# Performance work log

Hardware: AMD Instinct MI355X
Metric: run time of the kernel (lower is better)

Reference implementation:

```python
import jax, jax.numpy as jnp
import numpy as np
from jax import lax

DIM = 64
NUM_EXPERTS = 6
TOP_K = 2
B, H, W = 8, 128, 128
DN = ('NCHW', 'OIHW', 'NCHW')


def setup_inputs() -> dict:
    key = jax.random.key(0)
    ks = jax.random.split(key, 8)
    s_in = 1.0 / np.sqrt(DIM * 9)
    s_r = 1.0 / np.sqrt(DIM)
    return {
        'x': jax.random.normal(ks[0], (B, DIM, H, W), jnp.float32),
        'router_w': jax.random.normal(ks[1], (NUM_EXPERTS, DIM), jnp.float32) * s_r,
        'router_b': jnp.zeros((NUM_EXPERTS,), jnp.float32),
        'expert_bias': jnp.zeros((NUM_EXPERTS,), jnp.float32),
        'w1': jax.random.normal(ks[2], (NUM_EXPERTS, DIM, DIM, 3, 3), jnp.float32) * s_in,
        'b1': jnp.zeros((NUM_EXPERTS, DIM), jnp.float32),
        'w2': jax.random.normal(ks[3], (NUM_EXPERTS, DIM, DIM, 3, 3), jnp.float32) * s_in,
        'b2': jnp.zeros((NUM_EXPERTS, DIM), jnp.float32),
    }


def reference(x, router_w, router_b, expert_bias, w1, b1, w2, b2):
    # ---- router: global avg pool -> linear -> clamp -> +bias -> softmax ----
    pooled = x.mean(axis=(2, 3))                               # [B, C]
    logits = pooled @ router_w.T + router_b                    # [B, E]
    logits = jnp.clip(logits, -10.0, 10.0) + expert_bias[None, :]
    probs = jnp.clip(jax.nn.softmax(logits, axis=1), 1e-6, 1.0)
    top_v, top_i = lax.top_k(probs, TOP_K)                     # [B, K]
    top_v = top_v / (top_v.sum(axis=1, keepdims=True) + 1e-8)
    # per-sample combine weight for each expert: sum of top-k probs routed to it
    w_be = (jax.nn.one_hot(top_i, NUM_EXPERTS, dtype=x.dtype) * top_v[..., None]).sum(axis=1)  # [B, E]

    # ---- experts: Conv3x3 -> GELU -> Conv3x3, vmapped over expert dim ----
    def expert(w1e, b1e, w2e, b2e):
        h = lax.conv_general_dilated(x, w1e, (1, 1), 'SAME', dimension_numbers=DN)
        h = jax.nn.gelu(h + b1e[None, :, None, None])
        h = lax.conv_general_dilated(h, w2e, (1, 1), 'SAME', dimension_numbers=DN)
        return h + b2e[None, :, None, None]

    ys = jax.vmap(expert)(w1, b1, w2, b2)                      # [E, B, C, H, W]
    out = jnp.einsum('be,ebchw->bchw', w_be, ys)
    return out, jnp.zeros((), x.dtype)
```

## Files before the change

### kernel.cpp

```cpp
#include <hip/hip_runtime.h>
#include <hip/hip_bf16.h>
#include <cstdint>

typedef __attribute__((ext_vector_type(8))) short sh8;
typedef __attribute__((ext_vector_type(16))) float f32x16;
typedef unsigned short ushort_t;

#define HH 128
#define WW 128
#define HWSZ (HH*WW)
#define PW 130
#define PW64 (PW*64)
#define IMGSZ ((size_t)PW*PW*64)
#define WBEXP 36864

__device__ __forceinline__ float gelu_tanh(float x) {
    float u = 0.7978845608028654f * (x + 0.044715f * x * x * x);
    return 0.5f * x * (1.0f + tanhf(u));
}
__device__ __forceinline__ ushort_t f2b(float f) {
    __hip_bfloat16 h = __float2bfloat16(f);
    return *reinterpret_cast<ushort_t*>(&h);
}
__device__ __forceinline__ f32x16 mfma_bf16(sh8 a, sh8 b, f32x16 c) {
    return __builtin_amdgcn_mfma_f32_32x32x16_bf16(a, b, c, 0, 0, 0);
}

__global__ __launch_bounds__(256) void pool_kernel(const float* __restrict__ x,
                                                   float* __restrict__ pooled) {
    int bc = blockIdx.x;
    const float4* p4 = reinterpret_cast<const float4*>(x + (size_t)bc * HWSZ);
    float s = 0.f;
    for (int i = threadIdx.x; i < HWSZ / 4; i += 256) {
        float4 v = p4[i];
        s += (v.x + v.y) + (v.z + v.w);
    }
#pragma unroll
    for (int off = 32; off > 0; off >>= 1) s += __shfl_down(s, off, 64);
    __shared__ float red[4];
    if ((threadIdx.x & 63) == 0) red[threadIdx.x >> 6] = s;
    __syncthreads();
    if (threadIdx.x == 0)
        pooled[bc] = (red[0] + red[1] + red[2] + red[3]) * (1.0f / (float)HWSZ);
}

__global__ __launch_bounds__(64) void router_kernel(const float* __restrict__ pooled,
                                                    const float* __restrict__ rw,
                                                    const float* __restrict__ rb,
                                                    const float* __restrict__ eb,
                                                    const float* __restrict__ b2,
                                                    int* __restrict__ topi,
                                                    float* __restrict__ topw,
                                                    float* __restrict__ bsum,
                                                    float* __restrict__ outz) {
    __shared__ int sti[16];
    __shared__ float stw[16];
    int b = threadIdx.x;
    if (b == 8) outz[(size_t)8 * 64 * HWSZ] = 0.f;
    if (b < 8) {
        float lg[6];
        for (int e = 0; e < 6; ++e) {
            float s = rb[e];
            for (int c = 0; c < 64; ++c) s += pooled[b * 64 + c] * rw[e * 64 + c];
            lg[e] = fminf(fmaxf(s, -10.f), 10.f) + eb[e];
        }
        float m = lg[0];
        for (int e = 1; e < 6; ++e) m = fmaxf(m, lg[e]);
        float den = 0.f, pr[6];
        for (int e = 0; e < 6; ++e) { pr[e] = expf(lg[e] - m); den += pr[e]; }
        float inv = 1.0f / den;
        for (int e = 0; e < 6; ++e) pr[e] = fminf(fmaxf(pr[e] * inv, 1e-6f), 1.0f);
        int i0 = 0; float v0 = pr[0];
        for (int e = 1; e < 6; ++e) if (pr[e] > v0) { v0 = pr[e]; i0 = e; }
        int i1 = -1; float v1 = -1.f;
        for (int e = 0; e < 6; ++e) { if (e == i0) continue; if (pr[e] > v1) { v1 = pr[e]; i1 = e; } }
        float s2 = v0 + v1 + 1e-8f;
        topi[b * 2 + 0] = i0; topi[b * 2 + 1] = i1;
        topw[b * 2 + 0] = v0 / s2; topw[b * 2 + 1] = v1 / s2;
        sti[b * 2 + 0] = i0; sti[b * 2 + 1] = i1;
        stw[b * 2 + 0] = v0 / s2; stw[b * 2 + 1] = v1 / s2;
    }
    __syncthreads();
    for (int i = threadIdx.x; i < 512; i += 64) {
        int bb = i >> 6, c = i & 63;
        bsum[i] = stw[bb * 2] * b2[sti[bb * 2] * 64 + c] +
                  stw[bb * 2 + 1] * b2[sti[bb * 2 + 1] * 64 + c];
    }
}

__global__ __launch_bounds__(256) void convx_kernel(const float* __restrict__ x,
                                                    ushort_t* __restrict__ xp) {
    __shared__ ushort_t lt[128][72];
    int b = blockIdx.x >> 7, h = blockIdx.x & 127;
    int tid = threadIdx.x;
#pragma unroll
    for (int k = 0; k < 8; ++k) {
        int idx = tid + k * 256;
        int ci = idx >> 5, wg = idx & 31;
        float4 v = *reinterpret_cast<const float4*>(
            x + ((size_t)b * 64 + ci) * HWSZ + (size_t)h * WW + wg * 4);
        lt[wg * 4 + 0][ci] = f2b(v.x);
        lt[wg * 4 + 1][ci] = f2b(v.y);
        lt[wg * 4 + 2][ci] = f2b(v.z);
        lt[wg * 4 + 3][ci] = f2b(v.w);
    }
    __syncthreads();
    int w = tid >> 1, half = tid & 1;
    const int4* src = reinterpret_cast<const int4*>(&lt[w][half * 32]);
    int4 a0 = src[0], a1 = src[1], a2 = src[2], a3 = src[3];
    int4* dst = reinterpret_cast<int4*>(
        xp + (((size_t)b * PW + (h + 1)) * PW + (w + 1)) * 64 + half * 32);
    dst[0] = a0; dst[1] = a1; dst[2] = a2; dst[3] = a3;
}

__global__ __launch_bounds__(256) void convw1_kernel(const float* __restrict__ w1,
                                                     ushort_t* __restrict__ wb1f) {
    int blk = blockIdx.x;
    int e = blk / 9, t = blk - e * 9;
    for (int idx = threadIdx.x; idx < 4096; idx += 256) {
        int kc = idx >> 10, n = (idx >> 9) & 1, l = (idx >> 3) & 63, j = idx & 7;
        int co = n * 32 + (l & 31);
        int ci = kc * 16 + (l >> 5) * 8 + j;
        wb1f[(size_t)e * WBEXP + t * 4096 + idx] =
            f2b(w1[(((size_t)e * 64 + co) * 64 + ci) * 9 + t]);
    }
}

__global__ __launch_bounds__(256) void convw2_kernel(const float* __restrict__ w2,
                                                     const int* __restrict__ topi,
                                                     const float* __restrict__ topw,
                                                     ushort_t* __restrict__ wb2f) {
    int blk = blockIdx.x;
    int bs = blk / 9, t = blk - bs * 9;
    int e = topi[bs];
    float cw = topw[bs];
    for (int idx = threadIdx.x; idx < 4096; idx += 256) {
        int kc = idx >> 10, n = (idx >> 9) & 1, l = (idx >> 3) & 63, j = idx & 7;
        int co = n * 32 + (l & 31);
        int ci = kc * 16 + (l >> 5) * 8 + j;
        wb2f[(size_t)bs * WBEXP + t * 4096 + idx] =
            f2b(cw * w2[(((size_t)e * 64 + co) * 64 + ci) * 9 + t]);
    }
}

__global__ __launch_bounds__(256) void halo_kernel(ushort_t* __restrict__ buf) {
    ushort_t* p = buf + (size_t)blockIdx.x * IMGSZ;
    int tid = threadIdx.x;
    int4 z = make_int4(0, 0, 0, 0);
    for (int i = tid; i < 1040; i += 256) {
        reinterpret_cast<int4*>(p)[i] = z;
        reinterpret_cast<int4*>(p + (size_t)129 * PW64)[i] = z;
    }
    for (int i = tid; i < 128 * 8; i += 256) {
        int row = 1 + (i >> 3), j = i & 7;
        reinterpret_cast<int4*>(p + (size_t)row * PW64)[j] = z;
        reinterpret_cast<int4*>(p + ((size_t)row * PW + 129) * 64)[j] = z;
    }
}

__global__ __launch_bounds__(256) void conv1_mfma(const ushort_t* __restrict__ xp,
                                                  const ushort_t* __restrict__ wb1f,
                                                  const float* __restrict__ b1,
                                                  const int* __restrict__ topi,
                                                  ushort_t* __restrict__ hp,
                                                  int nslots, int slot0) {
    const int z = blockIdx.z;
    const int b = z / nslots, sl = z - b * nslots, s = slot0 + sl;
    const int e = topi[b * 2 + s];
    const int tid = threadIdx.x, l = tid & 63, wid = tid >> 6;
    const int n = wid & 1, rp = wid >> 1;
    const int hgrp = blockIdx.x >> 2, w0 = (blockIdx.x & 3) * 32;
    const int l31 = l & 31, lh = l >> 5;
    const int h0 = hgrp * 8 + rp * 4;

    const ushort_t* wbW = wb1f + (size_t)e * WBEXP + n * 512 + l * 8;
    const ushort_t* aB = xp + (size_t)b * IMGSZ + (size_t)h0 * PW64 +
                         (size_t)w0 * 64 + l31 * 64 + lh * 8;

    f32x16 acc0, acc1, acc2, acc3;
#pragma unroll
    for (int k2 = 0; k2 < 16; ++k2) { acc0[k2] = 0.f; acc1[k2] = 0.f; acc2[k2] = 0.f; acc3[k2] = 0.f; }

#pragma unroll
    for (int dr = 0; dr < 3; ++dr) {
        const ushort_t* ar = aB + (size_t)dr * PW64;
#pragma unroll
        for (int dc = 0; dc < 3; ++dc) {
            const ushort_t* ap = ar + dc * 64;
            const int t = dr * 3 + dc;
#pragma unroll
            for (int kc = 0; kc < 4; ++kc) {
                sh8 bf = *reinterpret_cast<const sh8*>(wbW + ((size_t)(t * 4 + kc)) * 1024);
                sh8 a0 = *reinterpret_cast<const sh8*>(ap + kc * 16);
                sh8 a1 = *reinterpret_cast<const sh8*>(ap + PW64 + kc * 16);
                sh8 a2 = *reinterpret_cast<const sh8*>(ap + 2 * PW64 + kc * 16);
                sh8 a3 = *reinterpret_cast<const sh8*>(ap + 3 * PW64 + kc * 16);
                acc0 = mfma_bf16(a0, bf, acc0);
                acc1 = mfma_bf16(a1, bf, acc1);
                acc2 = mfma_bf16(a2, bf, acc2);
                acc3 = mfma_bf16(a3, bf, acc3);
            }
        }
    }

    const float bv = b1[e * 64 + n * 32 + l31];
    const size_t ob0 = (((size_t)(sl * 8 + b) * PW + (h0 + 1)) * PW + (w0 + 1)) * 64 + n * 32 + l31;
#pragma unroll
    for (int i = 0; i < 4; ++i) {
        f32x16 a = (i == 0) ? acc0 : (i == 1) ? acc1 : (i == 2) ? acc2 : acc3;
        const size_t ob = ob0 + (size_t)i * PW64;
#pragma unroll
        for (int r = 0; r < 16; ++r) {
            int px = (r & 3) + 8 * (r >> 2) + 4 * lh;
            hp[ob + (size_t)px * 64] = f2b(gelu_tanh(a[r] + bv));
        }
    }
}

__global__ __launch_bounds__(256) void conv2_mfma(const ushort_t* __restrict__ hp,
                                                  const ushort_t* __restrict__ wb2f,
                                                  const float* __restrict__ bsum,
                                                  float* __restrict__ outF,
                                                  int s0, int s1, int addmode) {
    __shared__ float lt[4][32][33];
    const int b = blockIdx.z;
    const int tid = threadIdx.x, l = tid & 63, wid = tid >> 6;
    const int n = wid & 1, rp = wid >> 1;
    const int hgrp = blockIdx.x >> 2, w0 = (blockIdx.x & 3) * 32;
    const int l31 = l & 31, lh = l >> 5;
    const int h0 = hgrp * 4 + rp * 2;

    f32x16 acc0, acc1;
#pragma unroll
    for (int k2 = 0; k2 < 16; ++k2) { acc0[k2] = 0.f; acc1[k2] = 0.f; }

    for (int s = s0; s <= s1; ++s) {
        const ushort_t* wbW = wb2f + (size_t)(b * 2 + s) * WBEXP + n * 512 + l * 8;
        const ushort_t* aB = hp + (size_t)((s - s0) * 8 + b) * IMGSZ + (size_t)h0 * PW64 +
                             (size_t)w0 * 64 + l31 * 64 + lh * 8;
#pragma unroll
        for (int dr = 0; dr < 3; ++dr) {
            const ushort_t* ar = aB + (size_t)dr * PW64;
#pragma unroll
            for (int dc = 0; dc < 3; ++dc) {
                const ushort_t* ap = ar + dc * 64;
                const int t = dr * 3 + dc;
#pragma unroll
                for (int kc = 0; kc < 4; ++kc) {
                    sh8 bf = *reinterpret_cast<const sh8*>(wbW + ((size_t)(t * 4 + kc)) * 1024);
                    sh8 a0 = *reinterpret_cast<const sh8*>(ap + kc * 16);
                    sh8 a1 = *reinterpret_cast<const sh8*>(ap + PW64 + kc * 16);
                    acc0 = mfma_bf16(a0, bf, acc0);
                    acc1 = mfma_bf16(a1, bf, acc1);
                }
            }
        }
    }

    const float bq = addmode ? 0.f : bsum[b * 64 + n * 32 + l31];
#pragma unroll
    for (int i = 0; i < 2; ++i) {
        f32x16 a = i ? acc1 : acc0;
        const int h = h0 + i;
#pragma unroll
        for (int r = 0; r < 16; ++r) {
            int px = (r & 3) + 8 * (r >> 2) + 4 * lh;
            lt[wid][px][l31] = a[r] + bq;
        }
        const int q = lh, co = l31;
        const size_t ob = ((size_t)(b * 64 + n * 32 + co)) * HWSZ + (size_t)h * WW + w0 + q * 16;
#pragma unroll
        for (int v = 0; v < 4; ++v) {
            float o0 = lt[wid][q * 16 + v * 4 + 0][co];
            float o1 = lt[wid][q * 16 + v * 4 + 1][co];
            float o2 = lt[wid][q * 16 + v * 4 + 2][co];
            float o3 = lt[wid][q * 16 + v * 4 + 3][co];
            float4* dst = reinterpret_cast<float4*>(outF + ob + v * 4);
            if (addmode) {
                float4 pv = *dst;
                o0 += pv.x; o1 += pv.y; o2 += pv.z; o3 += pv.w;
            }
            float4 o; o.x = o0; o.y = o1; o.z = o2; o.w = o3;
            *dst = o;
        }
    }
}

extern "C" void kernel_launch(void* const* d_in, const int* in_sizes, int n_in,
                              void* d_out, int out_size, void* d_ws, size_t ws_size,
                              hipStream_t stream) {
    const float* x  = (const float*)d_in[0];
    const float* rw = (const float*)d_in[1];
    const float* rb = (const float*)d_in[2];
    const float* eb = (const float*)d_in[3];
    const float* w1 = (const float*)d_in[4];
    const float* b1 = (const float*)d_in[5];
    const float* w2 = (const float*)d_in[6];
    const float* b2 = (const float*)d_in[7];
    float* out = (float*)d_out;

    char* ws = (char*)d_ws;
    float*    pooled = (float*)(ws + 0);
    int*      topi   = (int*)(ws + 2048);
    float*    topw   = (float*)(ws + 2112);
    float*    bsum   = (float*)(ws + 2176);
    ushort_t* wb1f   = (ushort_t*)(ws + 4352);
    ushort_t* wb2f   = (ushort_t*)(ws + 446720);
    ushort_t* xp     = (ushort_t*)(ws + 1626368);
    ushort_t* hp     = (ushort_t*)(ws + 18931968);

    const bool two = ws_size >= 53543168ull;

    hipLaunchKernelGGL(pool_kernel, dim3(512), dim3(256), 0, stream, x, pooled);
    hipLaunchKernelGGL(router_kernel, dim3(1), dim3(64), 0, stream,
                       pooled, rw, rb, eb, b2, topi, topw, bsum, out);
    hipLaunchKernelGGL(convx_kernel, dim3(1024), dim3(256), 0, stream, x, xp);
    hipLaunchKernelGGL(convw1_kernel, dim3(54), dim3(256), 0, stream, w1, wb1f);
    hipLaunchKernelGGL(convw2_kernel, dim3(144), dim3(256), 0, stream, w2, topi, topw, wb2f);
    hipLaunchKernelGGL(halo_kernel, dim3(8), dim3(256), 0, stream, xp);
    hipLaunchKernelGGL(halo_kernel, dim3(two ? 16 : 8), dim3(256), 0, stream, hp);

    if (two) {
        hipLaunchKernelGGL(conv1_mfma, dim3(64, 1, 16), dim3(256), 0, stream,
                           xp, wb1f, b1, topi, hp, 2, 0);
        hipLaunchKernelGGL(conv2_mfma, dim3(128, 1, 8), dim3(256), 0, stream,
                           hp, wb2f, bsum, out, 0, 1, 0);
    } else {
        hipLaunchKernelGGL(conv1_mfma, dim3(64, 1, 8), dim3(256), 0, stream,
                           xp, wb1f, b1, topi, hp, 1, 0);
        hipLaunchKernelGGL(conv2_mfma, dim3(128, 1, 8), dim3(256), 0, stream,
                           hp, wb2f, bsum, out, 0, 0, 0);
        hipLaunchKernelGGL(conv1_mfma, dim3(64, 1, 8), dim3(256), 0, stream,
                           xp, wb1f, b1, topi, hp, 1, 1);
        hipLaunchKernelGGL(conv2_mfma, dim3(128, 1, 8), dim3(256), 0, stream,
                           hp, wb2f, bsum, out, 1, 1, 1);
    }
}
```

Baseline: 256.4 us.

## Fuse pooling into bf16 conversion, software-pipeline MFMA loads, merge halo kernels

Removes the separate pooling pass by accumulating channel sums with shuffles and atomics inside the bf16 conversion kernel, so x is read once fewer times. The router now applies the 1/HW scale itself. Both conv kernels get a 3-deep register prefetch pipeline over the 36 (or 72) MFMA steps, with launch_bounds occupancy hints. Conv1 is retiled from 4 rows to 2 rows per wave with twice the grid, and the two halo launches are merged into one. The changes trade atomics and possibly higher register pressure for fewer passes over memory and better latency hiding.

```diff
diff --git a/kernel.cpp b/kernel.cpp
--- a/kernel.cpp
+++ b/kernel.cpp
@@ -24,24 +24,6 @@
 }
 __device__ __forceinline__ f32x16 mfma_bf16(sh8 a, sh8 b, f32x16 c) {
     return __builtin_amdgcn_mfma_f32_32x32x16_bf16(a, b, c, 0, 0, 0);
-}
-
-__global__ __launch_bounds__(256) void pool_kernel(const float* __restrict__ x,
-                                                   float* __restrict__ pooled) {
-    int bc = blockIdx.x;
-    const float4* p4 = reinterpret_cast<const float4*>(x + (size_t)bc * HWSZ);
-    float s = 0.f;
-    for (int i = threadIdx.x; i < HWSZ / 4; i += 256) {
-        float4 v = p4[i];
-        s += (v.x + v.y) + (v.z + v.w);
-    }
-#pragma unroll
-    for (int off = 32; off > 0; off >>= 1) s += __shfl_down(s, off, 64);
-    __shared__ float red[4];
-    if ((threadIdx.x & 63) == 0) red[threadIdx.x >> 6] = s;
-    __syncthreads();
-    if (threadIdx.x == 0)
-        pooled[bc] = (red[0] + red[1] + red[2] + red[3]) * (1.0f / (float)HWSZ);
 }
 
 __global__ __launch_bounds__(64) void router_kernel(const float* __restrict__ pooled,
@@ -60,8 +42,9 @@
     if (b < 8) {
         float lg[6];
         for (int e = 0; e < 6; ++e) {
-            float s = rb[e];
+            float s = 0.f;
             for (int c = 0; c < 64; ++c) s += pooled[b * 64 + c] * rw[e * 64 + c];
+            s = s * (1.0f / (float)HWSZ) + rb[e];
             lg[e] = fminf(fmaxf(s, -10.f), 10.f) + eb[e];
         }
         float m = lg[0];
@@ -89,7 +72,8 @@
 }
 
 __global__ __launch_bounds__(256) void convx_kernel(const float* __restrict__ x,
-                                                    ushort_t* __restrict__ xp) {
+                                                    ushort_t* __restrict__ xp,
+                                                    float* __restrict__ pooled) {
     __shared__ ushort_t lt[128][72];
     int b = blockIdx.x >> 7, h = blockIdx.x & 127;
     int tid = threadIdx.x;
@@ -103,6 +87,10 @@
         lt[wg * 4 + 1][ci] = f2b(v.y);
         lt[wg * 4 + 2][ci] = f2b(v.z);
         lt[wg * 4 + 3][ci] = f2b(v.w);
+        float s4 = (v.x + v.y) + (v.z + v.w);
+#pragma unroll
+        for (int m = 16; m > 0; m >>= 1) s4 += __shfl_xor(s4, m, 64);
+        if ((tid & 31) == 0) atomicAdd(pooled + b * 64 + ci, s4);
     }
     __syncthreads();
     int w = tid >> 1, half = tid & 1;
@@ -143,8 +131,10 @@
     }
 }
 
-__global__ __launch_bounds__(256) void halo_kernel(ushort_t* __restrict__ buf) {
-    ushort_t* p = buf + (size_t)blockIdx.x * IMGSZ;
+__global__ __launch_bounds__(256) void halo_kernel(ushort_t* __restrict__ xp,
+                                                   ushort_t* __restrict__ hp) {
+    int img = blockIdx.x;
+    ushort_t* p = (img < 8) ? (xp + (size_t)img * IMGSZ) : (hp + (size_t)(img - 8) * IMGSZ);
     int tid = threadIdx.x;
     int4 z = make_int4(0, 0, 0, 0);
     for (int i = tid; i < 1040; i += 256) {
@@ -158,12 +148,12 @@
     }
 }
 
-__global__ __launch_bounds__(256) void conv1_mfma(const ushort_t* __restrict__ xp,
-                                                  const ushort_t* __restrict__ wb1f,
-                                                  const float* __restrict__ b1,
-                                                  const int* __restrict__ topi,
-                                                  ushort_t* __restrict__ hp,
-                                                  int nslots, int slot0) {
+__global__ __launch_bounds__(256, 4) void conv1_mfma(const ushort_t* __restrict__ xp,
+                                                     const ushort_t* __restrict__ wb1f,
+                                                     const float* __restrict__ b1,
+                                                     const int* __restrict__ topi,
+                                                     ushort_t* __restrict__ hp,
+                                                     int nslots, int slot0) {
     const int z = blockIdx.z;
     const int b = z / nslots, sl = z - b * nslots, s = slot0 + sl;
     const int e = topi[b * 2 + s];
@@ -171,43 +161,44 @@
     const int n = wid & 1, rp = wid >> 1;
     const int hgrp = blockIdx.x >> 2, w0 = (blockIdx.x & 3) * 32;
     const int l31 = l & 31, lh = l >> 5;
-    const int h0 = hgrp * 8 + rp * 4;
-
-    const ushort_t* wbW = wb1f + (size_t)e * WBEXP + n * 512 + l * 8;
+    const int h0 = hgrp * 4 + rp * 2;
+
     const ushort_t* aB = xp + (size_t)b * IMGSZ + (size_t)h0 * PW64 +
                          (size_t)w0 * 64 + l31 * 64 + lh * 8;
-
-    f32x16 acc0, acc1, acc2, acc3;
-#pragma unroll
-    for (int k2 = 0; k2 < 16; ++k2) { acc0[k2] = 0.f; acc1[k2] = 0.f; acc2[k2] = 0.f; acc3[k2] = 0.f; }
-
-#pragma unroll
-    for (int dr = 0; dr < 3; ++dr) {
-        const ushort_t* ar = aB + (size_t)dr * PW64;
-#pragma unroll
-        for (int dc = 0; dc < 3; ++dc) {
-            const ushort_t* ap = ar + dc * 64;
-            const int t = dr * 3 + dc;
-#pragma unroll
-            for (int kc = 0; kc < 4; ++kc) {
-                sh8 bf = *reinterpret_cast<const sh8*>(wbW + ((size_t)(t * 4 + kc)) * 1024);
-                sh8 a0 = *reinterpret_cast<const sh8*>(ap + kc * 16);
-                sh8 a1 = *reinterpret_cast<const sh8*>(ap + PW64 + kc * 16);
-                sh8 a2 = *reinterpret_cast<const sh8*>(ap + 2 * PW64 + kc * 16);
-                sh8 a3 = *reinterpret_cast<const sh8*>(ap + 3 * PW64 + kc * 16);
-                acc0 = mfma_bf16(a0, bf, acc0);
-                acc1 = mfma_bf16(a1, bf, acc1);
-                acc2 = mfma_bf16(a2, bf, acc2);
-                acc3 = mfma_bf16(a3, bf, acc3);
-            }
-        }
+    const ushort_t* wB = wb1f + (size_t)e * WBEXP + n * 512 + l * 8;
+
+    f32x16 acc0, acc1;
+#pragma unroll
+    for (int k2 = 0; k2 < 16; ++k2) { acc0[k2] = 0.f; acc1[k2] = 0.f; }
+
+    sh8 bA0[4], bA1[4], bB[4];
+#pragma unroll
+    for (int it = 0; it < 3; ++it) {
+        const int t = it >> 2, kc = it & 3, dr = t / 3, dc = t - dr * 3;
+        const ushort_t* ap = aB + (size_t)dr * PW64 + dc * 64 + kc * 16;
+        bA0[it] = *reinterpret_cast<const sh8*>(ap);
+        bA1[it] = *reinterpret_cast<const sh8*>(ap + PW64);
+        bB[it]  = *reinterpret_cast<const sh8*>(wB + t * 4096 + kc * 1024);
+    }
+#pragma unroll
+    for (int it = 0; it < 36; ++it) {
+        if (it + 3 < 36) {
+            const int jt = it + 3;
+            const int t = jt >> 2, kc = jt & 3, dr = t / 3, dc = t - dr * 3;
+            const ushort_t* ap = aB + (size_t)dr * PW64 + dc * 64 + kc * 16;
+            bA0[jt & 3] = *reinterpret_cast<const sh8*>(ap);
+            bA1[jt & 3] = *reinterpret_cast<const sh8*>(ap + PW64);
+            bB[jt & 3]  = *reinterpret_cast<const sh8*>(wB + t * 4096 + kc * 1024);
+        }
+        acc0 = mfma_bf16(bA0[it & 3], bB[it & 3], acc0);
+        acc1 = mfma_bf16(bA1[it & 3], bB[it & 3], acc1);
     }
 
     const float bv = b1[e * 64 + n * 32 + l31];
     const size_t ob0 = (((size_t)(sl * 8 + b) * PW + (h0 + 1)) * PW + (w0 + 1)) * 64 + n * 32 + l31;
 #pragma unroll
-    for (int i = 0; i < 4; ++i) {
-        f32x16 a = (i == 0) ? acc0 : (i == 1) ? acc1 : (i == 2) ? acc2 : acc3;
+    for (int i = 0; i < 2; ++i) {
+        f32x16 a = i ? acc1 : acc0;
         const size_t ob = ob0 + (size_t)i * PW64;
 #pragma unroll
         for (int r = 0; r < 16; ++r) {
@@ -217,11 +208,12 @@
     }
 }
 
-__global__ __launch_bounds__(256) void conv2_mfma(const ushort_t* __restrict__ hp,
-                                                  const ushort_t* __restrict__ wb2f,
-                                                  const float* __restrict__ bsum,
-                                                  float* __restrict__ outF,
-                                                  int s0, int s1, int addmode) {
+template <int NS>
+__global__ __launch_bounds__(256, 4) void conv2_mfma(const ushort_t* __restrict__ hp,
+                                                     const ushort_t* __restrict__ wb2f,
+                                                     const float* __restrict__ bsum,
+                                                     float* __restrict__ outF,
+                                                     int s0, int addmode) {
     __shared__ float lt[4][32][33];
     const int b = blockIdx.z;
     const int tid = threadIdx.x, l = tid & 63, wid = tid >> 6;
@@ -230,31 +222,38 @@
     const int l31 = l & 31, lh = l >> 5;
     const int h0 = hgrp * 4 + rp * 2;
 
+    const ushort_t* aB = hp + (size_t)b * IMGSZ + (size_t)h0 * PW64 +
+                         (size_t)w0 * 64 + l31 * 64 + lh * 8;
+    const ushort_t* wB = wb2f + (size_t)(b * 2 + s0) * WBEXP + n * 512 + l * 8;
+
+    constexpr int NIT = NS * 36;
     f32x16 acc0, acc1;
 #pragma unroll
     for (int k2 = 0; k2 < 16; ++k2) { acc0[k2] = 0.f; acc1[k2] = 0.f; }
 
-    for (int s = s0; s <= s1; ++s) {
-        const ushort_t* wbW = wb2f + (size_t)(b * 2 + s) * WBEXP + n * 512 + l * 8;
-        const ushort_t* aB = hp + (size_t)((s - s0) * 8 + b) * IMGSZ + (size_t)h0 * PW64 +
-                             (size_t)w0 * 64 + l31 * 64 + lh * 8;
-#pragma unroll
-        for (int dr = 0; dr < 3; ++dr) {
-            const ushort_t* ar = aB + (size_t)dr * PW64;
-#pragma unroll
-            for (int dc = 0; dc < 3; ++dc) {
-                const ushort_t* ap = ar + dc * 64;
-                const int t = dr * 3 + dc;
-#pragma unroll
-                for (int kc = 0; kc < 4; ++kc) {
-                    sh8 bf = *reinterpret_cast<const sh8*>(wbW + ((size_t)(t * 4 + kc)) * 1024);
-                    sh8 a0 = *reinterpret_cast<const sh8*>(ap + kc * 16);
-                    sh8 a1 = *reinterpret_cast<const sh8*>(ap + PW64 + kc * 16);
-                    acc0 = mfma_bf16(a0, bf, acc0);
-                    acc1 = mfma_bf16(a1, bf, acc1);
-                }
-            }
-        }
+    sh8 bA0[4], bA1[4], bB[4];
+#pragma unroll
+    for (int it = 0; it < 3; ++it) {
+        const int si = it / 36, r = it - si * 36;
+        const int t = r >> 2, kc = r & 3, dr = t / 3, dc = t - dr * 3;
+        const ushort_t* ap = aB + (size_t)si * 8 * IMGSZ + (size_t)dr * PW64 + dc * 64 + kc * 16;
+        bA0[it] = *reinterpret_cast<const sh8*>(ap);
+        bA1[it] = *reinterpret_cast<const sh8*>(ap + PW64);
+        bB[it]  = *reinterpret_cast<const sh8*>(wB + (size_t)si * WBEXP + t * 4096 + kc * 1024);
+    }
+#pragma unroll
+    for (int it = 0; it < NIT; ++it) {
+        if (it + 3 < NIT) {
+            const int jt = it + 3;
+            const int si = jt / 36, r = jt - si * 36;
+            const int t = r >> 2, kc = r & 3, dr = t / 3, dc = t - dr * 3;
+            const ushort_t* ap = aB + (size_t)si * 8 * IMGSZ + (size_t)dr * PW64 + dc * 64 + kc * 16;
+            bA0[jt & 3] = *reinterpret_cast<const sh8*>(ap);
+            bA1[jt & 3] = *reinterpret_cast<const sh8*>(ap + PW64);
+            bB[jt & 3]  = *reinterpret_cast<const sh8*>(wB + (size_t)si * WBEXP + t * 4096 + kc * 1024);
+        }
+        acc0 = mfma_bf16(bA0[it & 3], bB[it & 3], acc0);
+        acc1 = mfma_bf16(bA1[it & 3], bB[it & 3], acc1);
     }
 
     const float bq = addmode ? 0.f : bsum[b * 64 + n * 32 + l31];
@@ -311,28 +310,27 @@
 
     const bool two = ws_size >= 53543168ull;
 
-    hipLaunchKernelGGL(pool_kernel, dim3(512), dim3(256), 0, stream, x, pooled);
+    hipMemsetAsync(pooled, 0, 512 * sizeof(float), stream);
+    hipLaunchKernelGGL(convx_kernel, dim3(1024), dim3(256), 0, stream, x, xp, pooled);
     hipLaunchKernelGGL(router_kernel, dim3(1), dim3(64), 0, stream,
                        pooled, rw, rb, eb, b2, topi, topw, bsum, out);
-    hipLaunchKernelGGL(convx_kernel, dim3(1024), dim3(256), 0, stream, x, xp);
     hipLaunchKernelGGL(convw1_kernel, dim3(54), dim3(256), 0, stream, w1, wb1f);
     hipLaunchKernelGGL(convw2_kernel, dim3(144), dim3(256), 0, stream, w2, topi, topw, wb2f);
-    hipLaunchKernelGGL(halo_kernel, dim3(8), dim3(256), 0, stream, xp);
-    hipLaunchKernelGGL(halo_kernel, dim3(two ? 16 : 8), dim3(256), 0, stream, hp);
+    hipLaunchKernelGGL(halo_kernel, dim3(two ? 24 : 16), dim3(256), 0, stream, xp, hp);
 
     if (two) {
-        hipLaunchKernelGGL(conv1_mfma, dim3(64, 1, 16), dim3(256), 0, stream,
+        hipLaunchKernelGGL(conv1_mfma, dim3(128, 1, 16), dim3(256), 0, stream,
                            xp, wb1f, b1, topi, hp, 2, 0);
-        hipLaunchKernelGGL(conv2_mfma, dim3(128, 1, 8), dim3(256), 0, stream,
-                           hp, wb2f, bsum, out, 0, 1, 0);
+        hipLaunchKernelGGL((conv2_mfma<2>), dim3(128, 1, 8), dim3(256), 0, stream,
+                           hp, wb2f, bsum, out, 0, 0);
     } else {
-        hipLaunchKernelGGL(conv1_mfma, dim3(64, 1, 8), dim3(256), 0, stream,
+        hipLaunchKernelGGL(conv1_mfma, dim3(128, 1, 8), dim3(256), 0, stream,
                            xp, wb1f, b1, topi, hp, 1, 0);
-        hipLaunchKernelGGL(conv2_mfma, dim3(128, 1, 8), dim3(256), 0, stream,
-                           hp, wb2f, bsum, out, 0, 0, 0);
-        hipLaunchKernelGGL(conv1_mfma, dim3(64, 1, 8), dim3(256), 0, stream,
+        hipLaunchKernelGGL((conv2_mfma<1>), dim3(128, 1, 8), dim3(256), 0, stream,
+                           hp, wb2f, bsum, out, 0, 0);
+        hipLaunchKernelGGL(conv1_mfma, dim3(128, 1, 8), dim3(256), 0, stream,
                            xp, wb1f, b1, topi, hp, 1, 1);
-        hipLaunchKernelGGL(conv2_mfma, dim3(128, 1, 8), dim3(256), 0, stream,
-                           hp, wb2f, bsum, out, 1, 1, 1);
-    }
-}
+        hipLaunchKernelGGL((conv2_mfma<1>), dim3(128, 1, 8), dim3(256), 0, stream,
+                           hp, wb2f, bsum, out, 1, 1);
+    }
+}
```

Result: slower. 274.4 us (+7.0%).
